# Performance work log

Hardware: AMD Instinct MI355X
Metric: run time of the kernel (lower is better)

## Reference

```python
import jax, jax.numpy as jnp
import numpy as np

MARGIN = 1.0

def setup_inputs() -> dict:
    key = jax.random.key(0)
    k1, k2 = jax.random.split(key)
    B, D, NUM_CLASSES = 4096, 512, 64
    inputs = jax.random.normal(k1, (B, D), dtype=jnp.float32)
    labels = jax.random.randint(k2, (B,), 0, NUM_CLASSES, dtype=jnp.int64)
    return {"inputs": inputs, "labels": labels}

def reference(inputs, labels):
    # Full pairwise squared L2 distances via the ||a-b||^2 = ||a||^2 + ||b||^2 - 2 a.b expansion
    sq = jnp.sum(inputs * inputs, axis=1)                      # [B]
    d2 = sq[:, None] + sq[None, :] - 2.0 * (inputs @ inputs.T)  # [B, B]
    d2 = jnp.maximum(d2, 0.0)
    # Safe sqrt: zero (self) distances get exactly 0 without NaN-producing sqrt(0) grads
    nz = d2 > 1e-12
    dist = jnp.where(nz, jnp.sqrt(jnp.where(nz, d2, 1.0)), 0.0)  # [B, B]

    mask = labels[:, None] == labels[None, :]                   # [B, B] same-class mask (includes self)
    mask_f = mask.astype(dist.dtype)

    # Per-anchor: mean distance to positives (self included, contributing 0, as in the torch loop)
    ap_mean = jnp.sum(dist * mask_f, axis=1) / jnp.sum(mask_f, axis=1)  # [B]
    # Per-anchor: min distance to negatives
    an_min = jnp.min(jnp.where(mask, jnp.inf, dist), axis=1)            # [B]

    tmp = ap_mean - an_min + MARGIN                             # [B]
    # `if tmp > 0: loss += tmp` over the batch == sum of relu(tmp)
    return jnp.sum(jnp.maximum(tmp, 0.0))
```

## Files before the change

kernel.cpp:

```cpp
#include <hip/hip_runtime.h>
#include <hip/hip_bf16.h>

typedef unsigned short u16;
typedef unsigned int u32;
typedef __attribute__((ext_vector_type(8))) short short8;
typedef __attribute__((ext_vector_type(8))) u16 ushort8;
typedef __attribute__((ext_vector_type(4))) float f32x4;

#define B_SZ 4096
#define D_SZ 512
#define NCLS 64
#define NT   32
#define NBLK (NT * (NT + 1) / 2)


__device__ __forceinline__ u16 f2bf(float x) {
    union { float f; u32 u; } a; a.f = x;
    u32 r = a.u + 0x7fffu + ((a.u >> 16) & 1u);
    return (u16)(r >> 16);
}

__device__ __forceinline__ void gload16(const void* g, void* l) {
    __builtin_amdgcn_global_load_lds(
        (const __attribute__((address_space(1))) u32*)g,
        (__attribute__((address_space(3))) u32*)l,
        16, 0, 0);
}


__global__ __launch_bounds__(256) void prep_kernel(
    const float* __restrict__ in, u16* __restrict__ bfout,
    float* __restrict__ sq, float* __restrict__ ap_sum, u32* __restrict__ an_min)
{
    const int wave = threadIdx.x >> 6, l = threadIdx.x & 63;
    const int row = blockIdx.x * 4 + wave;
    const float* p = in + (size_t)row * D_SZ + l * 8;
    float4 v0 = *(const float4*)p;
    float4 v1 = *(const float4*)(p + 4);
    float s = v0.x*v0.x + v0.y*v0.y + v0.z*v0.z + v0.w*v0.w
            + v1.x*v1.x + v1.y*v1.y + v1.z*v1.z + v1.w*v1.w;
    ushort8 o;
    o[0]=f2bf(v0.x); o[1]=f2bf(v0.y); o[2]=f2bf(v0.z); o[3]=f2bf(v0.w);
    o[4]=f2bf(v1.x); o[5]=f2bf(v1.y); o[6]=f2bf(v1.z); o[7]=f2bf(v1.w);
    *(ushort8*)(bfout + (size_t)row * D_SZ + l * 8) = o;
    #pragma unroll
    for (int off = 1; off < 64; off <<= 1) s += __shfl_xor(s, off);
    if (l == 0) {
        sq[row] = s;
        ap_sum[row] = 0.0f;
        an_min[row] = 0x7f800000u;
    }
}


__global__ __launch_bounds__(256) void tile_kernel(
    const u16* __restrict__ bfin, const int* __restrict__ lab,
    const float* __restrict__ sq, float* __restrict__ ap_sum, u32* __restrict__ an_min)
{
    __shared__ u16 As[128 * 32];
    __shared__ u16 Bs[128 * 32];
    __shared__ float sqA[128], sqB[128];
    __shared__ int labA[128], labB[128];

    const int t = threadIdx.x;

    const int bid = blockIdx.x;
    int tm = (int)((__builtin_sqrtf(8.0f * (float)bid + 1.0f) - 1.0f) * 0.5f);
    while ((tm + 1) * (tm + 2) / 2 <= bid) ++tm;
    while (tm * (tm + 1) / 2 > bid) --tm;
    const int tn = bid - tm * (tm + 1) / 2;
    const bool diag = (tm == tn);

    const int rowBase = tm * 128;
    const int colBase = tn * 128;

    if (t < 128) { labA[t] = lab[rowBase + t]; sqA[t] = sq[rowBase + t]; }
    else { int u = t - 128; labB[u] = lab[colBase + u]; sqB[u] = sq[colBase + u]; }

    const int wave = t >> 6, lane = t & 63;
    const int wr = wave >> 1, wc = wave & 1;
    const int g = lane >> 4, c = lane & 15;

    f32x4 acc[4][4];
    #pragma unroll
    for (int i = 0; i < 4; ++i)
        #pragma unroll
        for (int j = 0; j < 4; ++j)
            acc[i][j] = (f32x4){0.f, 0.f, 0.f, 0.f};

    const u16* gA = bfin + (size_t)(rowBase + (t >> 2)) * D_SZ + (t & 3) * 8;
    const u16* gB = bfin + (size_t)(colBase + (t >> 2)) * D_SZ + (t & 3) * 8;

    #pragma unroll 1
    for (int kk = 0; kk < D_SZ / 32; ++kk) {
        gload16(gA + kk * 32,             As + t * 8);
        gload16(gA + kk * 32 + 64 * D_SZ, As + 2048 + t * 8);
        gload16(gB + kk * 32,             Bs + t * 8);
        gload16(gB + kk * 32 + 64 * D_SZ, Bs + 2048 + t * 8);
        __syncthreads();

        short8 a[4], b[4];
        #pragma unroll
        for (int mi = 0; mi < 4; ++mi)
            a[mi] = *(const short8*)&As[(wr * 64 + mi * 16 + c) * 32 + g * 8];
        #pragma unroll
        for (int ni = 0; ni < 4; ++ni)
            b[ni] = *(const short8*)&Bs[(wc * 64 + ni * 16 + c) * 32 + g * 8];

        #pragma unroll
        for (int mi = 0; mi < 4; ++mi)
            #pragma unroll
            for (int ni = 0; ni < 4; ++ni)
                acc[mi][ni] = __builtin_amdgcn_mfma_f32_16x16x32_bf16(a[mi], b[ni], acc[mi][ni], 0, 0, 0);
        __syncthreads();
    }

    float sc[4], mc[4];
    #pragma unroll
    for (int ni = 0; ni < 4; ++ni) { sc[ni] = 0.0f; mc[ni] = __builtin_inff(); }

    #pragma unroll
    for (int mi = 0; mi < 4; ++mi) {
        #pragma unroll
        for (int r = 0; r < 4; ++r) {
            const int lrow = wr * 64 + mi * 16 + g * 4 + r;
            const int i = rowBase + lrow;
            const int li = labA[lrow];
            const float sqi = sqA[lrow];
            float s = 0.0f;
            float mn = __builtin_inff();
            #pragma unroll
            for (int ni = 0; ni < 4; ++ni) {
                const int lcol = wc * 64 + ni * 16 + c;
                float d2 = sqi + sqB[lcol] - 2.0f * acc[mi][ni][r];
                d2 = fmaxf(d2, 0.0f);
                float dist = (d2 > 1e-12f) ? __builtin_sqrtf(d2) : 0.0f;
                if (diag && lrow == lcol) dist = 0.0f;
                if (li == labB[lcol]) { s += dist; sc[ni] += dist; }
                else                  { mn = fminf(mn, dist); mc[ni] = fminf(mc[ni], dist); }
            }
            #pragma unroll
            for (int off = 1; off < 16; off <<= 1) {
                s += __shfl_xor(s, off);
                mn = fminf(mn, __shfl_xor(mn, off));
            }
            if (c == 0) {
                atomicAdd(&ap_sum[i], s);
                atomicMin(&an_min[i], __float_as_uint(mn));
            }
        }
    }

    if (!diag) {
        #pragma unroll
        for (int ni = 0; ni < 4; ++ni) {
            float s = sc[ni], mn = mc[ni];
            s += __shfl_xor(s, 16); s += __shfl_xor(s, 32);
            mn = fminf(mn, __shfl_xor(mn, 16)); mn = fminf(mn, __shfl_xor(mn, 32));
            if (lane < 16) {
                const int j = colBase + wc * 64 + ni * 16 + c;
                atomicAdd(&ap_sum[j], s);
                atomicMin(&an_min[j], __float_as_uint(mn));
            }
        }
    }
}


__global__ __launch_bounds__(1024) void final_kernel(
    const float* __restrict__ ap_sum, const u32* __restrict__ an_min,
    const int* __restrict__ lab, float* __restrict__ out)
{
    __shared__ int cnt[NCLS];
    __shared__ float wsum[16];
    const int t = threadIdx.x;
    if (t < NCLS) cnt[t] = 0;
    __syncthreads();
    for (int i = t; i < B_SZ; i += 1024) atomicAdd(&cnt[lab[i]], 1);
    __syncthreads();
    float v = 0.0f;
    for (int i = t; i < B_SZ; i += 1024) {
        float apm = ap_sum[i] / (float)cnt[lab[i]];
        float anm = __uint_as_float(an_min[i]);
        v += fmaxf(apm - anm + 1.0f, 0.0f);
    }
    #pragma unroll
    for (int off = 1; off < 64; off <<= 1) v += __shfl_xor(v, off);
    if ((t & 63) == 0) wsum[t >> 6] = v;
    __syncthreads();
    if (t == 0) {
        float s = 0.0f;
        #pragma unroll
        for (int w = 0; w < 16; ++w) s += wsum[w];
        out[0] = s;
    }
}


extern "C" void kernel_launch(void* const* d_in, const int* in_sizes, int n_in,
                              void* d_out, int out_size, void* d_ws, size_t ws_size,
                              hipStream_t stream) {
    const float* inputs = (const float*)d_in[0];
    const int* labels = (const int*)d_in[1];
    float* out = (float*)d_out;

    char* ws = (char*)d_ws;
    float* ap_sum = (float*)ws;
    u32* an_min = (u32*)(ws + 16384);
    float* sq = (float*)(ws + 32768);
    u16* bfin = (u16*)(ws + 65536);

    prep_kernel<<<dim3(B_SZ / 4), dim3(256), 0, stream>>>(inputs, bfin, sq, ap_sum, an_min);
    tile_kernel<<<dim3(NBLK), dim3(256), 0, stream>>>(bfin, labels, sq, ap_sum, an_min);
    final_kernel<<<dim3(1), dim3(1024), 0, stream>>>(ap_sum, an_min, labels, out);
}
```

Before: 43.65 us.

## Double-buffer swizzled K tiles, reuse A tile on diagonal, fuse final reduction

The GEMM K-loop now uses BK=64 with double-buffered LDS tiles loaded asynchronously one step ahead, plus an XOR swizzle to avoid LDS bank conflicts. Diagonal blocks load only the A tile and reuse it as B. The separate final kernel is removed: the last tile block to finish, found through an atomic counter, computes the loss. This saves a launch and half the sync barriers, at the cost of more LDS per block and possibly lower occupancy.

```diff
diff --git a/kernel.cpp b/kernel.cpp
--- a/kernel.cpp
+++ b/kernel.cpp
@@ -10,8 +10,10 @@
 #define B_SZ 4096
 #define D_SZ 512
 #define NCLS 64
+#define BK   64
 #define NT   32
 #define NBLK (NT * (NT + 1) / 2)
+#define TILE_ELEMS (128 * BK)
 
 
 __device__ __forceinline__ u16 f2bf(float x) {
@@ -27,11 +29,21 @@
         16, 0, 0);
 }
 
+__device__ __forceinline__ void stage_tile(const u16* __restrict__ gsrc, u16* dst, int t) {
+    const int r = t >> 3;
+    const int col = ((t & 7) ^ (r & 7)) << 3;
+    #pragma unroll
+    for (int q = 0; q < 4; ++q)
+        gload16(gsrc + (size_t)(q * 32 + r) * D_SZ + col, dst + q * 2048 + t * 8);
+}
+
 
 __global__ __launch_bounds__(256) void prep_kernel(
     const float* __restrict__ in, u16* __restrict__ bfout,
-    float* __restrict__ sq, float* __restrict__ ap_sum, u32* __restrict__ an_min)
+    float* __restrict__ sq, float* __restrict__ ap_sum, u32* __restrict__ an_min,
+    int* __restrict__ done)
 {
+    if (blockIdx.x == 0 && threadIdx.x == 0) *done = 0;
     const int wave = threadIdx.x >> 6, l = threadIdx.x & 63;
     const int row = blockIdx.x * 4 + wave;
     const float* p = in + (size_t)row * D_SZ + l * 8;
@@ -53,14 +65,21 @@
 }
 
 
+extern __shared__ char smem[];
+
 __global__ __launch_bounds__(256) void tile_kernel(
     const u16* __restrict__ bfin, const int* __restrict__ lab,
-    const float* __restrict__ sq, float* __restrict__ ap_sum, u32* __restrict__ an_min)
+    const float* __restrict__ sq, float* __restrict__ ap_sum, u32* __restrict__ an_min,
+    int* __restrict__ done, float* __restrict__ out)
 {
-    __shared__ u16 As[128 * 32];
-    __shared__ u16 Bs[128 * 32];
-    __shared__ float sqA[128], sqB[128];
-    __shared__ int labA[128], labB[128];
+    float* sqA = (float*)smem;
+    float* sqB = sqA + 128;
+    int*   labA = (int*)(smem + 1024);
+    int*   labB = labA + 128;
+    u16*   As = (u16*)(smem + 2048);
+    u16*   Bs = As + 2 * TILE_ELEMS;
+    __shared__ int isLast;
+    __shared__ float wsum[4];
 
     const int t = threadIdx.x;
 
@@ -88,30 +107,39 @@
         for (int j = 0; j < 4; ++j)
             acc[i][j] = (f32x4){0.f, 0.f, 0.f, 0.f};
 
-    const u16* gA = bfin + (size_t)(rowBase + (t >> 2)) * D_SZ + (t & 3) * 8;
-    const u16* gB = bfin + (size_t)(colBase + (t >> 2)) * D_SZ + (t & 3) * 8;
+    const u16* gA = bfin + (size_t)rowBase * D_SZ;
+    const u16* gB = bfin + (size_t)colBase * D_SZ;
+
+    stage_tile(gA, As, t);
+    if (!diag) stage_tile(gB, Bs, t);
+    __syncthreads();
 
     #pragma unroll 1
-    for (int kk = 0; kk < D_SZ / 32; ++kk) {
-        gload16(gA + kk * 32,             As + t * 8);
-        gload16(gA + kk * 32 + 64 * D_SZ, As + 2048 + t * 8);
-        gload16(gB + kk * 32,             Bs + t * 8);
-        gload16(gB + kk * 32 + 64 * D_SZ, Bs + 2048 + t * 8);
-        __syncthreads();
-
-        short8 a[4], b[4];
-        #pragma unroll
-        for (int mi = 0; mi < 4; ++mi)
-            a[mi] = *(const short8*)&As[(wr * 64 + mi * 16 + c) * 32 + g * 8];
-        #pragma unroll
-        for (int ni = 0; ni < 4; ++ni)
-            b[ni] = *(const short8*)&Bs[(wc * 64 + ni * 16 + c) * 32 + g * 8];
-
-        #pragma unroll
-        for (int mi = 0; mi < 4; ++mi)
+    for (int kk = 0; kk < D_SZ / BK; ++kk) {
+        const int cur = kk & 1;
+        if (kk + 1 < D_SZ / BK) {
+            stage_tile(gA + (kk + 1) * BK, As + (cur ^ 1) * TILE_ELEMS, t);
+            if (!diag) stage_tile(gB + (kk + 1) * BK, Bs + (cur ^ 1) * TILE_ELEMS, t);
+        }
+        const u16* abuf = As + cur * TILE_ELEMS;
+        const u16* bbuf = diag ? abuf : Bs + cur * TILE_ELEMS;
+
+        #pragma unroll
+        for (int ks = 0; ks < 2; ++ks) {
+            const int sw = (((ks << 2) + g) ^ (c & 7)) << 3;
+            short8 a[4], b[4];
+            #pragma unroll
+            for (int mi = 0; mi < 4; ++mi)
+                a[mi] = *(const short8*)&abuf[(wr * 64 + mi * 16 + c) * BK + sw];
             #pragma unroll
             for (int ni = 0; ni < 4; ++ni)
-                acc[mi][ni] = __builtin_amdgcn_mfma_f32_16x16x32_bf16(a[mi], b[ni], acc[mi][ni], 0, 0, 0);
+                b[ni] = *(const short8*)&bbuf[(wc * 64 + ni * 16 + c) * BK + sw];
+            #pragma unroll
+            for (int mi = 0; mi < 4; ++mi)
+                #pragma unroll
+                for (int ni = 0; ni < 4; ++ni)
+                    acc[mi][ni] = __builtin_amdgcn_mfma_f32_16x16x32_bf16(a[mi], b[ni], acc[mi][ni], 0, 0, 0);
+        }
         __syncthreads();
     }
 
@@ -164,36 +192,33 @@
             }
         }
     }
-}
-
-
-__global__ __launch_bounds__(1024) void final_kernel(
-    const float* __restrict__ ap_sum, const u32* __restrict__ an_min,
-    const int* __restrict__ lab, float* __restrict__ out)
-{
-    __shared__ int cnt[NCLS];
-    __shared__ float wsum[16];
-    const int t = threadIdx.x;
+
+    __threadfence();
+    if (t == 0) {
+        int old = atomicAdd(done, 1);
+        isLast = (old == NBLK - 1) ? 1 : 0;
+    }
+    __syncthreads();
+    if (!isLast) return;
+
+    int* cnt = labA;
     if (t < NCLS) cnt[t] = 0;
     __syncthreads();
-    for (int i = t; i < B_SZ; i += 1024) atomicAdd(&cnt[lab[i]], 1);
+    for (int i = t; i < B_SZ; i += 256) atomicAdd(&cnt[lab[i]], 1);
     __syncthreads();
     float v = 0.0f;
-    for (int i = t; i < B_SZ; i += 1024) {
-        float apm = ap_sum[i] / (float)cnt[lab[i]];
-        float anm = __uint_as_float(an_min[i]);
+    for (int i = t; i < B_SZ; i += 256) {
+        float apv = atomicAdd(&ap_sum[i], 0.0f);
+        u32 mnb = atomicMin(&an_min[i], 0x7f800000u);
+        float apm = apv / (float)cnt[lab[i]];
+        float anm = __uint_as_float(mnb);
         v += fmaxf(apm - anm + 1.0f, 0.0f);
     }
     #pragma unroll
     for (int off = 1; off < 64; off <<= 1) v += __shfl_xor(v, off);
     if ((t & 63) == 0) wsum[t >> 6] = v;
     __syncthreads();
-    if (t == 0) {
-        float s = 0.0f;
-        #pragma unroll
-        for (int w = 0; w < 16; ++w) s += wsum[w];
-        out[0] = s;
-    }
+    if (t == 0) out[0] = wsum[0] + wsum[1] + wsum[2] + wsum[3];
 }
 
 
@@ -208,9 +233,11 @@
     float* ap_sum = (float*)ws;
     u32* an_min = (u32*)(ws + 16384);
     float* sq = (float*)(ws + 32768);
+    int* done = (int*)(ws + 49152);
     u16* bfin = (u16*)(ws + 65536);
 
-    prep_kernel<<<dim3(B_SZ / 4), dim3(256), 0, stream>>>(inputs, bfin, sq, ap_sum, an_min);
-    tile_kernel<<<dim3(NBLK), dim3(256), 0, stream>>>(bfin, labels, sq, ap_sum, an_min);
-    final_kernel<<<dim3(1), dim3(1024), 0, stream>>>(ap_sum, an_min, labels, out);
-}
+    const int smem_bytes = 2048 + 4 * TILE_ELEMS * (int)sizeof(u16);
+
+    prep_kernel<<<dim3(B_SZ / 4), dim3(256), 0, stream>>>(inputs, bfin, sq, ap_sum, an_min, done);
+    tile_kernel<<<dim3(NBLK), dim3(256), smem_bytes, stream>>>(bfin, labels, sq, ap_sum, an_min, done, out);
+}
```

New measurement: 118.0 us. 2.7x slower.
